# Performance work log

Measured on AMD Instinct MI355X. Metric: run time of the kernel, lower is better.

Reference implementation:

```python
import jax, jax.numpy as jnp
import numpy as np

N = 50000   # nodes
E = 600000  # edges
F = 128     # num_features
H = 128     # hidden_channels
G = 64      # graphs in batch


def setup_inputs() -> dict:
    key = jax.random.key(0)
    ks = jax.random.split(key, 12)
    x = jax.random.normal(ks[0], (N, F), dtype=jnp.float32)
    edge_index = jax.random.randint(ks[1], (2, E), 0, N, dtype=jnp.int64)
    edge_mask = jax.random.randint(ks[2], (E,), 0, 3, dtype=jnp.int64)
    batch = jnp.sort(jax.random.randint(ks[3], (N,), 0, G, dtype=jnp.int64))
    s = 0.05
    W1 = jax.random.normal(ks[4], (F, H), dtype=jnp.float32) * s
    b1 = jnp.zeros((H,), jnp.float32)
    W2 = jax.random.normal(ks[5], (H, H), dtype=jnp.float32) * s
    b2 = jnp.zeros((H,), jnp.float32)
    W3 = jax.random.normal(ks[6], (H, H), dtype=jnp.float32) * s
    b3 = jnp.zeros((H,), jnp.float32)
    Wl = jax.random.normal(ks[7], (H, 1), dtype=jnp.float32) * s
    bl = jnp.zeros((1,), jnp.float32)
    return {"x": x, "edge_index": edge_index, "edge_mask": edge_mask, "batch": batch,
            "W1": W1, "b1": b1, "W2": W2, "b2": b2, "W3": W3, "b3": b3, "Wl": Wl, "bl": bl}


def gcn_conv(x, W, b, src, dst, ew, n):
    """PyG GCNConv: add self-loops, symmetric deg^-1/2 normalization.
    ew is a {0,1} per-edge weight implementing the dynamic edge subset
    (equivalent to edge_index[:, idx] subsetting, since masked edges
    contribute neither to degree nor to aggregation)."""
    h = x @ W                                                # [n, H]
    deg = jax.ops.segment_sum(ew, dst, num_segments=n) + 1.0  # self-loop adds 1
    dinv = jax.lax.rsqrt(deg)                                # deg^-1/2
    norm = ew * dinv[src] * dinv[dst]                        # per-edge coeff
    agg = jax.ops.segment_sum(h[src] * norm[:, None], dst, num_segments=n)
    agg = agg + h * (dinv * dinv)[:, None]                   # self-loop term 1/deg_i
    return agg + b


def reference(x, edge_index, edge_mask, batch, W1, b1, W2, b2, W3, b3, Wl, bl):
    src, dst = edge_index[0], edge_index[1]
    ones = jnp.ones((E,), x.dtype)
    h = jax.nn.relu(gcn_conv(x, W1, b1, src, dst, ones, N))
    m1 = (edge_mask == 1).astype(x.dtype)
    h = jax.nn.relu(gcn_conv(h, W2, b2, src, dst, m1, N))
    m2 = (edge_mask == 2).astype(x.dtype)
    h = gcn_conv(h, W3, b3, src, dst, m2, N)
    # global_mean_pool over batch ids
    sums = jax.ops.segment_sum(h, batch, num_segments=G)        # [G, H]
    cnt = jax.ops.segment_sum(jnp.ones((N,), h.dtype), batch, num_segments=G)
    pooled = sums / jnp.clip(cnt, 1.0)[:, None]
    # dropout(p=0.3) is identity in eval mode
    return pooled @ Wl + bl
```

## Files before the change

kernel.cpp:

```cpp
#include <hip/hip_runtime.h>

#define NN 50000
#define EE 600000
#define HH 128
#define GG 64
#define NPAD 50176
#define NR 196
#define RN 256
#define EPB 3072
#define SCAP 3584
#define STAGB 7168
#define SC12 1536
#define CSR1OFF 702464
#define CSR2OFF 1003520

typedef __attribute__((ext_vector_type(8))) short short8;
typedef __attribute__((ext_vector_type(4))) float f32x4;
typedef __attribute__((ext_vector_type(4))) unsigned int u32x4;

__device__ __forceinline__ float bf2f(unsigned int u16) {
    union { unsigned int i; float f; } v; v.i = u16 << 16; return v.f;
}
__device__ __forceinline__ unsigned short f2bf(float f) {
    union { float f; unsigned int i; } v; v.f = f;
    unsigned int u = v.i;
    return (unsigned short)((u + 0x7FFFu + ((u >> 16) & 1u)) >> 16);
}

__device__ __forceinline__ short8 cvt8(f32x4 lo, f32x4 hi) {
    short8 r;
    r[0] = (short)f2bf(lo[0]); r[1] = (short)f2bf(lo[1]);
    r[2] = (short)f2bf(lo[2]); r[3] = (short)f2bf(lo[3]);
    r[4] = (short)f2bf(hi[0]); r[5] = (short)f2bf(hi[1]);
    r[6] = (short)f2bf(hi[2]); r[7] = (short)f2bf(hi[3]);
    return r;
}

__global__ void k_wt3z(const float* __restrict__ W1, const float* __restrict__ W2,
                       const float* __restrict__ W3, unsigned short* __restrict__ wt,
                       float* __restrict__ sums, int* __restrict__ scnt) {
    int i = blockIdx.x * 256 + threadIdx.x;
    if (i < GG * HH) sums[i] = 0.f;
    if (i < NR) scnt[i] = 0;
    int which = i >> 14;
    int r = i & 16383;
    const float* w = (which == 0) ? W1 : (which == 1) ? W2 : W3;
    int k = r >> 7, n = r & 127;
    wt[which * 16384 + n * HH + k] = f2bf(w[r]);
}

__global__ __launch_bounds__(256) void k_part(const int* __restrict__ ei, const int* __restrict__ mask,
                                              int* __restrict__ scnt, unsigned int* __restrict__ sbuf) {
    __shared__ int bcnt[256];
    __shared__ int bcur[256];
    __shared__ int gbase[256];
    int t = threadIdx.x;
    int e0 = blockIdx.x * EPB;
    unsigned int pk[12]; int bin[12];
    bcnt[t] = 0; bcur[t] = 0;
    __syncthreads();
    #pragma unroll
    for (int j = 0; j < 12; j++) {
        int e = e0 + j * 256 + t;
        if (e < EE) {
            int s = ei[e];
            int d = ei[EE + e];
            int m = mask[e];
            pk[j] = (unsigned int)s | ((unsigned int)(d & 255) << 16) | ((unsigned int)m << 24);
            bin[j] = d >> 8;
            atomicAdd(&bcnt[bin[j]], 1);
        } else bin[j] = -1;
    }
    __syncthreads();
    int v = bcnt[t];
    gbase[t] = (v > 0) ? atomicAdd(&scnt[t], v) : 0;
    __syncthreads();
    #pragma unroll
    for (int j = 0; j < 12; j++) {
        if (bin[j] >= 0) {
            int b = bin[j];
            int pos = gbase[b] + atomicAdd(&bcur[b], 1);
            if (pos < SCAP) sbuf[(size_t)b * SCAP + pos] = pk[j];
        }
    }
}

__global__ __launch_bounds__(256) void k_bld(const int* __restrict__ scnt,
                                             const unsigned int* __restrict__ sbuf,
                                             float* __restrict__ dinv,
                                             int* __restrict__ rpS, int* __restrict__ rpE,
                                             unsigned short* __restrict__ csr) {
    __shared__ int l0[RN], l1[RN], l2[RN];
    __shared__ int lrp0[RN], lrp1[RN], lrp2[RN];
    __shared__ int lc0[RN], lc1[RN], lc2[RN];
    __shared__ int wsum[12];
    __shared__ int ctot[3];
    __shared__ unsigned short stag[STAGB];
    int t = threadIdx.x, lane = t & 63, w = t >> 6;
    int rng = blockIdx.x;
    l0[t] = 0; l1[t] = 0; l2[t] = 0;
    lc0[t] = 0; lc1[t] = 0; lc2[t] = 0;
    __syncthreads();
    int cnt = scnt[rng]; if (cnt > SCAP) cnt = SCAP;
    const unsigned int* sb = sbuf + (size_t)rng * SCAP;
    for (int i = t; i < cnt; i += 256) {
        unsigned int p = sb[i];
        int dl = (int)((p >> 16) & 255u);
        int m = (int)(p >> 24);
        atomicAdd(&l0[dl], 1);
        if (m == 1) atomicAdd(&l1[dl], 1);
        else if (m == 2) atomicAdd(&l2[dl], 1);
    }
    __syncthreads();
    int a = l0[t], b = l1[t], c = l2[t];
    int x0 = a, x1 = b, x2 = c;
    #pragma unroll
    for (int off = 1; off < 64; off <<= 1) {
        int u0 = __shfl_up(x0, off), u1 = __shfl_up(x1, off), u2 = __shfl_up(x2, off);
        if (lane >= off) { x0 += u0; x1 += u1; x2 += u2; }
    }
    if (lane == 63) { wsum[w] = x0; wsum[4 + w] = x1; wsum[8 + w] = x2; }
    __syncthreads();
    int wo0 = 0, wo1 = 0, wo2 = 0;
    for (int k = 0; k < w; k++) { wo0 += wsum[k]; wo1 += wsum[4 + k]; wo2 += wsum[8 + k]; }
    int e0 = wo0 + x0 - a, e1 = wo1 + x1 - b, e2 = wo2 + x2 - c;
    lrp0[t] = e0; lrp1[t] = e1; lrp2[t] = e2;
    if (t == 255) { ctot[0] = e0 + a; ctot[1] = e1 + b; ctot[2] = e2 + c; }
    int node = rng * RN + t;
    dinv[node] = rsqrtf((float)a + 1.0f);
    dinv[NPAD + node] = rsqrtf((float)b + 1.0f);
    dinv[2 * NPAD + node] = rsqrtf((float)c + 1.0f);
    int base0 = rng * SCAP;
    int base1 = CSR1OFF + rng * SC12;
    int base2 = CSR2OFF + rng * SC12;
    rpS[node] = base0 + e0;            rpE[node] = base0 + e0 + a;
    rpS[NPAD + node] = base1 + e1;     rpE[NPAD + node] = base1 + e1 + b;
    rpS[2 * NPAD + node] = base2 + e2; rpE[2 * NPAD + node] = base2 + e2 + c;
    __syncthreads();
    int c0 = ctot[0], c1 = ctot[1], c2 = ctot[2];
    for (int i = t; i < cnt; i += 256) {
        unsigned int p = sb[i];
        unsigned short src = (unsigned short)(p & 0xffffu);
        int dl = (int)((p >> 16) & 255u);
        int m = (int)(p >> 24);
        int sl = lrp0[dl] + atomicAdd(&lc0[dl], 1);
        stag[sl] = src;
        if (m == 1) { sl = c0 + lrp1[dl] + atomicAdd(&lc1[dl], 1); stag[sl] = src; }
        else if (m == 2) { sl = c0 + c1 + lrp2[dl] + atomicAdd(&lc2[dl], 1); stag[sl] = src; }
    }
    __syncthreads();
    for (int i = t; i < c0; i += 256) csr[base0 + i] = stag[i];
    for (int i = t; i < c1; i += 256) csr[base1 + i] = stag[c0 + i];
    for (int i = t; i < c2; i += 256) csr[base2 + i] = stag[c0 + c1 + i];
}

__global__ __launch_bounds__(256) void k_gemm_f(const float* __restrict__ in,
                                                const unsigned short* __restrict__ wt,
                                                const float* __restrict__ dinv,
                                                unsigned short* __restrict__ h) {
    int w = threadIdx.x >> 6, lane = threadIdx.x & 63;
    int lr = lane & 15, lg = lane >> 4;
    int rowbase = (blockIdx.x * 4 + w) * 16;
    if (rowbase >= NN) return;
    int arow = rowbase + lr;
    const f32x4* ap = (const f32x4*)(in + (size_t)arow * HH + lg * 8);
    short8 a0 = cvt8(ap[0], ap[1]);
    short8 a1 = cvt8(ap[8], ap[9]);
    short8 a2 = cvt8(ap[16], ap[17]);
    short8 a3 = cvt8(ap[24], ap[25]);
    f32x4 acc[8];
    #pragma unroll
    for (int i = 0; i < 8; i++) acc[i] = (f32x4){0.f, 0.f, 0.f, 0.f};
    const unsigned short* wbase = wt + lr * HH + lg * 8;
    #pragma unroll
    for (int nc = 0; nc < 8; nc++) {
        const short8* bp = (const short8*)(wbase + nc * 16 * HH);
        short8 b0 = bp[0], b1 = bp[4], b2 = bp[8], b3 = bp[12];
        acc[nc] = __builtin_amdgcn_mfma_f32_16x16x32_bf16(a0, b0, acc[nc], 0, 0, 0);
        acc[nc] = __builtin_amdgcn_mfma_f32_16x16x32_bf16(a1, b1, acc[nc], 0, 0, 0);
        acc[nc] = __builtin_amdgcn_mfma_f32_16x16x32_bf16(a2, b2, acc[nc], 0, 0, 0);
        acc[nc] = __builtin_amdgcn_mfma_f32_16x16x32_bf16(a3, b3, acc[nc], 0, 0, 0);
    }
    int orow = rowbase + lg * 4;
    f32x4 dv = *(const f32x4*)(dinv + orow);
    #pragma unroll
    for (int nc = 0; nc < 8; nc++) {
        #pragma unroll
        for (int j = 0; j < 4; j++) {
            h[(size_t)(orow + j) * HH + nc * 16 + lr] = f2bf(acc[nc][j] * dv[j]);
        }
    }
}

__global__ __launch_bounds__(256) void k_gemm_b(const unsigned short* __restrict__ in,
                                                const unsigned short* __restrict__ wt,
                                                const float* __restrict__ dinv,
                                                unsigned short* __restrict__ h) {
    int w = threadIdx.x >> 6, lane = threadIdx.x & 63;
    int lr = lane & 15, lg = lane >> 4;
    int rowbase = (blockIdx.x * 4 + w) * 16;
    if (rowbase >= NN) return;
    int arow = rowbase + lr;
    const short8* ap = (const short8*)(in + (size_t)arow * HH + lg * 8);
    short8 a0 = ap[0], a1 = ap[4], a2 = ap[8], a3 = ap[12];
    f32x4 acc[8];
    #pragma unroll
    for (int i = 0; i < 8; i++) acc[i] = (f32x4){0.f, 0.f, 0.f, 0.f};
    const unsigned short* wbase = wt + lr * HH + lg * 8;
    #pragma unroll
    for (int nc = 0; nc < 8; nc++) {
        const short8* bp = (const short8*)(wbase + nc * 16 * HH);
        short8 b0 = bp[0], b1 = bp[4], b2 = bp[8], b3 = bp[12];
        acc[nc] = __builtin_amdgcn_mfma_f32_16x16x32_bf16(a0, b0, acc[nc], 0, 0, 0);
        acc[nc] = __builtin_amdgcn_mfma_f32_16x16x32_bf16(a1, b1, acc[nc], 0, 0, 0);
        acc[nc] = __builtin_amdgcn_mfma_f32_16x16x32_bf16(a2, b2, acc[nc], 0, 0, 0);
        acc[nc] = __builtin_amdgcn_mfma_f32_16x16x32_bf16(a3, b3, acc[nc], 0, 0, 0);
    }
    int orow = rowbase + lg * 4;
    f32x4 dv = *(const f32x4*)(dinv + orow);
    #pragma unroll
    for (int nc = 0; nc < 8; nc++) {
        #pragma unroll
        for (int j = 0; j < 4; j++) {
            h[(size_t)(orow + j) * HH + nc * 16 + lr] = f2bf(acc[nc][j] * dv[j]);
        }
    }
}

__global__ __launch_bounds__(256) void k_agg(const unsigned short* __restrict__ h,
                                             const float* __restrict__ dinv,
                                             const unsigned short* __restrict__ csr,
                                             const int* __restrict__ rpS,
                                             const int* __restrict__ rpE,
                                             const float* __restrict__ bias,
                                             unsigned short* __restrict__ g,
                                             int relu) {
    int tid = threadIdx.x;
    int n = blockIdx.x * 16 + (tid >> 4);
    int l = tid & 15;
    u32x4 hv = *(const u32x4*)(h + (size_t)n * HH + l * 8);
    float acc[8];
    #pragma unroll
    for (int q = 0; q < 4; q++) {
        acc[2*q] = bf2f(hv[q] & 0xffffu);
        acc[2*q+1] = bf2f(hv[q] >> 16);
    }
    int e = rpS[n], end = rpE[n];
    for (; e + 7 < end; e += 8) {
        int s0 = (int)csr[e],     s1 = (int)csr[e + 1], s2 = (int)csr[e + 2], s3 = (int)csr[e + 3];
        int s4 = (int)csr[e + 4], s5 = (int)csr[e + 5], s6 = (int)csr[e + 6], s7 = (int)csr[e + 7];
        u32x4 v0 = *(const u32x4*)(h + (size_t)s0 * HH + l * 8);
        u32x4 v1 = *(const u32x4*)(h + (size_t)s1 * HH + l * 8);
        u32x4 v2 = *(const u32x4*)(h + (size_t)s2 * HH + l * 8);
        u32x4 v3 = *(const u32x4*)(h + (size_t)s3 * HH + l * 8);
        u32x4 v4 = *(const u32x4*)(h + (size_t)s4 * HH + l * 8);
        u32x4 v5 = *(const u32x4*)(h + (size_t)s5 * HH + l * 8);
        u32x4 v6 = *(const u32x4*)(h + (size_t)s6 * HH + l * 8);
        u32x4 v7 = *(const u32x4*)(h + (size_t)s7 * HH + l * 8);
        #pragma unroll
        for (int q = 0; q < 4; q++) {
            acc[2*q] += bf2f(v0[q] & 0xffffu); acc[2*q+1] += bf2f(v0[q] >> 16);
            acc[2*q] += bf2f(v1[q] & 0xffffu); acc[2*q+1] += bf2f(v1[q] >> 16);
            acc[2*q] += bf2f(v2[q] & 0xffffu); acc[2*q+1] += bf2f(v2[q] >> 16);
            acc[2*q] += bf2f(v3[q] & 0xffffu); acc[2*q+1] += bf2f(v3[q] >> 16);
            acc[2*q] += bf2f(v4[q] & 0xffffu); acc[2*q+1] += bf2f(v4[q] >> 16);
            acc[2*q] += bf2f(v5[q] & 0xffffu); acc[2*q+1] += bf2f(v5[q] >> 16);
            acc[2*q] += bf2f(v6[q] & 0xffffu); acc[2*q+1] += bf2f(v6[q] >> 16);
            acc[2*q] += bf2f(v7[q] & 0xffffu); acc[2*q+1] += bf2f(v7[q] >> 16);
        }
    }
    for (; e + 3 < end; e += 4) {
        int s0 = (int)csr[e], s1 = (int)csr[e + 1], s2 = (int)csr[e + 2], s3 = (int)csr[e + 3];
        u32x4 v0 = *(const u32x4*)(h + (size_t)s0 * HH + l * 8);
        u32x4 v1 = *(const u32x4*)(h + (size_t)s1 * HH + l * 8);
        u32x4 v2 = *(const u32x4*)(h + (size_t)s2 * HH + l * 8);
        u32x4 v3 = *(const u32x4*)(h + (size_t)s3 * HH + l * 8);
        #pragma unroll
        for (int q = 0; q < 4; q++) {
            acc[2*q] += bf2f(v0[q] & 0xffffu); acc[2*q+1] += bf2f(v0[q] >> 16);
            acc[2*q] += bf2f(v1[q] & 0xffffu); acc[2*q+1] += bf2f(v1[q] >> 16);
            acc[2*q] += bf2f(v2[q] & 0xffffu); acc[2*q+1] += bf2f(v2[q] >> 16);
            acc[2*q] += bf2f(v3[q] & 0xffffu); acc[2*q+1] += bf2f(v3[q] >> 16);
        }
    }
    for (; e < end; e++) {
        int s0 = (int)csr[e];
        u32x4 v0 = *(const u32x4*)(h + (size_t)s0 * HH + l * 8);
        #pragma unroll
        for (int q = 0; q < 4; q++) {
            acc[2*q] += bf2f(v0[q] & 0xffffu); acc[2*q+1] += bf2f(v0[q] >> 16);
        }
    }
    float di = dinv[n];
    f32x4 bp0 = *(const f32x4*)(bias + l * 8);
    f32x4 bp1 = *(const f32x4*)(bias + l * 8 + 4);
    float bb[8] = {bp0[0], bp0[1], bp0[2], bp0[3], bp1[0], bp1[1], bp1[2], bp1[3]};
    #pragma unroll
    for (int q = 0; q < 8; q++) {
        acc[q] = acc[q] * di + bb[q];
        if (relu) acc[q] = fmaxf(acc[q], 0.f);
    }
    u32x4 o;
    #pragma unroll
    for (int q = 0; q < 4; q++)
        o[q] = (unsigned int)f2bf(acc[2*q]) | ((unsigned int)f2bf(acc[2*q+1]) << 16);
    *(u32x4*)(g + (size_t)n * HH + l * 8) = o;
}

__global__ __launch_bounds__(128) void k_pool_part(const unsigned short* __restrict__ g3,
                                                   const int* __restrict__ batch,
                                                   float* __restrict__ sums) {
    int t = threadIdx.x;
    int n0 = blockIdx.x * 64;
    int n1 = n0 + 64; if (n1 > NN) n1 = NN;
    int curb = batch[n0];
    float acc = 0.f;
    for (int n = n0; n < n1; n++) {
        int b = batch[n];
        if (b != curb) {
            atomicAdd(&sums[curb * HH + t], acc);
            acc = 0.f;
            curb = b;
        }
        acc += bf2f((unsigned int)g3[(size_t)n * HH + t]);
    }
    atomicAdd(&sums[curb * HH + t], acc);
}

__device__ __forceinline__ int lbound(const int* a, int n, int key) {
    int lo = 0, hi = n;
    while (lo < hi) { int mid = (lo + hi) >> 1; if (a[mid] < key) lo = mid + 1; else hi = mid; }
    return lo;
}

__global__ __launch_bounds__(128) void k_head(const float* __restrict__ sums,
                                              const int* __restrict__ batch,
                                              const float* __restrict__ Wl,
                                              const float* __restrict__ bl,
                                              float* __restrict__ out) {
    int gid = blockIdx.x;
    int t = threadIdx.x;
    int lo = lbound(batch, NN, gid);
    int hi = lbound(batch, NN, gid + 1);
    float cnt = (float)(hi - lo);
    if (cnt < 1.f) cnt = 1.f;
    float prod = (sums[gid * HH + t] / cnt) * Wl[t];
    __shared__ float sm[128];
    sm[t] = prod;
    __syncthreads();
    for (int off = 64; off > 0; off >>= 1) {
        if (t < off) sm[t] += sm[t + off];
        __syncthreads();
    }
    if (t == 0) out[gid] = sm[0] + bl[0];
}

extern "C" void kernel_launch(void* const* d_in, const int* in_sizes, int n_in,
                              void* d_out, int out_size, void* d_ws, size_t ws_size,
                              hipStream_t stream) {
    const float* x    = (const float*)d_in[0];
    const int*   ei   = (const int*)d_in[1];
    const int*   mask = (const int*)d_in[2];
    const int*   batch= (const int*)d_in[3];
    const float* W1   = (const float*)d_in[4];
    const float* b1   = (const float*)d_in[5];
    const float* W2   = (const float*)d_in[6];
    const float* b2   = (const float*)d_in[7];
    const float* W3   = (const float*)d_in[8];
    const float* b3   = (const float*)d_in[9];
    const float* Wl   = (const float*)d_in[10];
    const float* bl   = (const float*)d_in[11];
    float* out = (float*)d_out;

    char* ws = (char*)d_ws;
    unsigned short* g = (unsigned short*)(ws + 0);
    unsigned short* h = (unsigned short*)(ws + 12800000);
    unsigned short* wt1 = (unsigned short*)(ws + 25600000);
    unsigned short* wt2 = wt1 + 16384;
    unsigned short* wt3 = wt2 + 16384;
    float* dinv= (float*)(ws + 25698304);
    int* rpS   = (int*)(ws + 26300416);
    int* rpE   = (int*)(ws + 26902528);
    int* scnt  = (int*)(ws + 27504640);
    unsigned short* csr = (unsigned short*)(ws + 27505664);
    unsigned int* sbuf = (unsigned int*)(ws + 30114816);
    float* sums = (float*)(ws + 32924672);

    float* dinv1 = dinv;
    float* dinv2 = dinv + NPAD;
    float* dinv3 = dinv + 2 * NPAD;

    dim3 b256(256);
    k_wt3z<<<dim3(192), b256, 0, stream>>>(W1, W2, W3, wt1, sums, scnt);
    k_part<<<dim3((EE + EPB - 1) / EPB), b256, 0, stream>>>(ei, mask, scnt, sbuf);
    k_bld<<<dim3(NR), b256, 0, stream>>>(scnt, sbuf, dinv, rpS, rpE, csr);

    dim3 ggrid((NN + 63) / 64);
    dim3 agrid(NN / 16);

    k_gemm_f<<<ggrid, b256, 0, stream>>>(x, wt1, dinv1, h);
    k_agg<<<agrid, b256, 0, stream>>>(h, dinv1, csr, rpS, rpE, b1, g, 1);
    k_gemm_b<<<ggrid, b256, 0, stream>>>(g, wt2, dinv2, h);
    k_agg<<<agrid, b256, 0, stream>>>(h, dinv2, csr, rpS + NPAD, rpE + NPAD, b2, g, 1);
    k_gemm_b<<<ggrid, b256, 0, stream>>>(g, wt3, dinv3, h);
    k_agg<<<agrid, b256, 0, stream>>>(h, dinv3, csr, rpS + 2 * NPAD, rpE + 2 * NPAD, b3, g, 0);

    k_pool_part<<<dim3((NN + 63) / 64), dim3(128), 0, stream>>>(g, batch, sums);
    k_head<<<dim3(GG), dim3(128), 0, stream>>>(sums, batch, Wl, bl, out);
}
```

Before: 182.5 us.

## Fuse aggregation with the following layer's GEMM via shared-memory tile

Layers 1 and 2 now aggregate neighbours, apply bias and ReLU, and stage the 16-row result in shared memory. The same block then runs the next layer's MFMA GEMM on that tile and writes the dinv-scaled output directly. This drops two separate GEMM launches and the round trip of the intermediate activation through global memory. The costs are a block barrier after the irregular gather phase, more shared memory per block, and a smaller GEMM tile per block, with W reloaded per block.

Measured after the change: 160.0 us (median of 2 runs). 12.3% less time.

```diff
diff --git a/kernel.cpp b/kernel.cpp
--- a/kernel.cpp
+++ b/kernel.cpp
@@ -13,6 +13,7 @@
 #define SC12 1536
 #define CSR1OFF 702464
 #define CSR2OFF 1003520
+#define GTS 138
 
 typedef __attribute__((ext_vector_type(8))) short short8;
 typedef __attribute__((ext_vector_type(4))) float f32x4;
@@ -192,60 +193,9 @@
     }
 }
 
-__global__ __launch_bounds__(256) void k_gemm_b(const unsigned short* __restrict__ in,
-                                                const unsigned short* __restrict__ wt,
-                                                const float* __restrict__ dinv,
-                                                unsigned short* __restrict__ h) {
-    int w = threadIdx.x >> 6, lane = threadIdx.x & 63;
-    int lr = lane & 15, lg = lane >> 4;
-    int rowbase = (blockIdx.x * 4 + w) * 16;
-    if (rowbase >= NN) return;
-    int arow = rowbase + lr;
-    const short8* ap = (const short8*)(in + (size_t)arow * HH + lg * 8);
-    short8 a0 = ap[0], a1 = ap[4], a2 = ap[8], a3 = ap[12];
-    f32x4 acc[8];
-    #pragma unroll
-    for (int i = 0; i < 8; i++) acc[i] = (f32x4){0.f, 0.f, 0.f, 0.f};
-    const unsigned short* wbase = wt + lr * HH + lg * 8;
-    #pragma unroll
-    for (int nc = 0; nc < 8; nc++) {
-        const short8* bp = (const short8*)(wbase + nc * 16 * HH);
-        short8 b0 = bp[0], b1 = bp[4], b2 = bp[8], b3 = bp[12];
-        acc[nc] = __builtin_amdgcn_mfma_f32_16x16x32_bf16(a0, b0, acc[nc], 0, 0, 0);
-        acc[nc] = __builtin_amdgcn_mfma_f32_16x16x32_bf16(a1, b1, acc[nc], 0, 0, 0);
-        acc[nc] = __builtin_amdgcn_mfma_f32_16x16x32_bf16(a2, b2, acc[nc], 0, 0, 0);
-        acc[nc] = __builtin_amdgcn_mfma_f32_16x16x32_bf16(a3, b3, acc[nc], 0, 0, 0);
-    }
-    int orow = rowbase + lg * 4;
-    f32x4 dv = *(const f32x4*)(dinv + orow);
-    #pragma unroll
-    for (int nc = 0; nc < 8; nc++) {
-        #pragma unroll
-        for (int j = 0; j < 4; j++) {
-            h[(size_t)(orow + j) * HH + nc * 16 + lr] = f2bf(acc[nc][j] * dv[j]);
-        }
-    }
-}
-
-__global__ __launch_bounds__(256) void k_agg(const unsigned short* __restrict__ h,
-                                             const float* __restrict__ dinv,
-                                             const unsigned short* __restrict__ csr,
-                                             const int* __restrict__ rpS,
-                                             const int* __restrict__ rpE,
-                                             const float* __restrict__ bias,
-                                             unsigned short* __restrict__ g,
-                                             int relu) {
-    int tid = threadIdx.x;
-    int n = blockIdx.x * 16 + (tid >> 4);
-    int l = tid & 15;
-    u32x4 hv = *(const u32x4*)(h + (size_t)n * HH + l * 8);
-    float acc[8];
-    #pragma unroll
-    for (int q = 0; q < 4; q++) {
-        acc[2*q] = bf2f(hv[q] & 0xffffu);
-        acc[2*q+1] = bf2f(hv[q] >> 16);
-    }
-    int e = rpS[n], end = rpE[n];
+__device__ __forceinline__ void agg_edges(const unsigned short* __restrict__ h,
+                                          const unsigned short* __restrict__ csr,
+                                          int e, int end, int l, float* acc) {
     for (; e + 7 < end; e += 8) {
         int s0 = (int)csr[e],     s1 = (int)csr[e + 1], s2 = (int)csr[e + 2], s3 = (int)csr[e + 3];
         int s4 = (int)csr[e + 4], s5 = (int)csr[e + 5], s6 = (int)csr[e + 6], s7 = (int)csr[e + 7];
@@ -291,19 +241,101 @@
             acc[2*q] += bf2f(v0[q] & 0xffffu); acc[2*q+1] += bf2f(v0[q] >> 16);
         }
     }
+}
+
+__global__ __launch_bounds__(256) void k_aggemm(const unsigned short* __restrict__ h,
+                                                const float* __restrict__ dinvA,
+                                                const unsigned short* __restrict__ csr,
+                                                const int* __restrict__ rpS,
+                                                const int* __restrict__ rpE,
+                                                const float* __restrict__ bias,
+                                                const unsigned short* __restrict__ wt,
+                                                const float* __restrict__ dinvB,
+                                                unsigned short* __restrict__ hout) {
+    __shared__ unsigned short gt[16][GTS];
+    int tid = threadIdx.x;
+    int n0 = blockIdx.x * 16;
+    int nl = tid >> 4;
+    int n = n0 + nl;
+    int l = tid & 15;
+    u32x4 hv = *(const u32x4*)(h + (size_t)n * HH + l * 8);
+    float acc[8];
+    #pragma unroll
+    for (int q = 0; q < 4; q++) {
+        acc[2*q] = bf2f(hv[q] & 0xffffu);
+        acc[2*q+1] = bf2f(hv[q] >> 16);
+    }
+    agg_edges(h, csr, rpS[n], rpE[n], l, acc);
+    float di = dinvA[n];
+    f32x4 bp0 = *(const f32x4*)(bias + l * 8);
+    f32x4 bp1 = *(const f32x4*)(bias + l * 8 + 4);
+    float bb[8] = {bp0[0], bp0[1], bp0[2], bp0[3], bp1[0], bp1[1], bp1[2], bp1[3]};
+    #pragma unroll
+    for (int q = 0; q < 8; q++) {
+        float v = fmaxf(acc[q] * di + bb[q], 0.f);
+        gt[nl][l * 8 + q] = f2bf(v);
+    }
+    __syncthreads();
+    int lane = tid & 63, w = tid >> 6;
+    int lr = lane & 15, lg = lane >> 4;
+    short8 a0 = *(const short8*)&gt[lr][lg * 8];
+    short8 a1 = *(const short8*)&gt[lr][32 + lg * 8];
+    short8 a2 = *(const short8*)&gt[lr][64 + lg * 8];
+    short8 a3 = *(const short8*)&gt[lr][96 + lg * 8];
+    f32x4 oacc[2];
+    oacc[0] = (f32x4){0.f, 0.f, 0.f, 0.f};
+    oacc[1] = (f32x4){0.f, 0.f, 0.f, 0.f};
+    #pragma unroll
+    for (int nc2 = 0; nc2 < 2; nc2++) {
+        int nc = w * 2 + nc2;
+        const short8* bp = (const short8*)(wt + (nc * 16 + lr) * HH + lg * 8);
+        short8 b0 = bp[0], b1 = bp[4], b2 = bp[8], b3 = bp[12];
+        oacc[nc2] = __builtin_amdgcn_mfma_f32_16x16x32_bf16(a0, b0, oacc[nc2], 0, 0, 0);
+        oacc[nc2] = __builtin_amdgcn_mfma_f32_16x16x32_bf16(a1, b1, oacc[nc2], 0, 0, 0);
+        oacc[nc2] = __builtin_amdgcn_mfma_f32_16x16x32_bf16(a2, b2, oacc[nc2], 0, 0, 0);
+        oacc[nc2] = __builtin_amdgcn_mfma_f32_16x16x32_bf16(a3, b3, oacc[nc2], 0, 0, 0);
+    }
+    int orow = n0 + lg * 4;
+    f32x4 dv = *(const f32x4*)(dinvB + orow);
+    #pragma unroll
+    for (int nc2 = 0; nc2 < 2; nc2++) {
+        int nc = w * 2 + nc2;
+        #pragma unroll
+        for (int j = 0; j < 4; j++) {
+            hout[(size_t)(orow + j) * HH + nc * 16 + lr] = f2bf(oacc[nc2][j] * dv[j]);
+        }
+    }
+}
+
+__global__ __launch_bounds__(256) void k_agg(const unsigned short* __restrict__ h,
+                                             const float* __restrict__ dinv,
+                                             const unsigned short* __restrict__ csr,
+                                             const int* __restrict__ rpS,
+                                             const int* __restrict__ rpE,
+                                             const float* __restrict__ bias,
+                                             unsigned short* __restrict__ g) {
+    int tid = threadIdx.x;
+    int n = blockIdx.x * 16 + (tid >> 4);
+    int l = tid & 15;
+    u32x4 hv = *(const u32x4*)(h + (size_t)n * HH + l * 8);
+    float acc[8];
+    #pragma unroll
+    for (int q = 0; q < 4; q++) {
+        acc[2*q] = bf2f(hv[q] & 0xffffu);
+        acc[2*q+1] = bf2f(hv[q] >> 16);
+    }
+    agg_edges(h, csr, rpS[n], rpE[n], l, acc);
     float di = dinv[n];
     f32x4 bp0 = *(const f32x4*)(bias + l * 8);
     f32x4 bp1 = *(const f32x4*)(bias + l * 8 + 4);
     float bb[8] = {bp0[0], bp0[1], bp0[2], bp0[3], bp1[0], bp1[1], bp1[2], bp1[3]};
-    #pragma unroll
-    for (int q = 0; q < 8; q++) {
-        acc[q] = acc[q] * di + bb[q];
-        if (relu) acc[q] = fmaxf(acc[q], 0.f);
-    }
     u32x4 o;
     #pragma unroll
-    for (int q = 0; q < 4; q++)
-        o[q] = (unsigned int)f2bf(acc[2*q]) | ((unsigned int)f2bf(acc[2*q+1]) << 16);
+    for (int q = 0; q < 4; q++) {
+        float v0 = acc[2*q] * di + bb[2*q];
+        float v1 = acc[2*q+1] * di + bb[2*q+1];
+        o[q] = (unsigned int)f2bf(v0) | ((unsigned int)f2bf(v1) << 16);
+    }
     *(u32x4*)(g + (size_t)n * HH + l * 8) = o;
 }
 
@@ -399,11 +431,9 @@
     dim3 agrid(NN / 16);
 
     k_gemm_f<<<ggrid, b256, 0, stream>>>(x, wt1, dinv1, h);
-    k_agg<<<agrid, b256, 0, stream>>>(h, dinv1, csr, rpS, rpE, b1, g, 1);
-    k_gemm_b<<<ggrid, b256, 0, stream>>>(g, wt2, dinv2, h);
-    k_agg<<<agrid, b256, 0, stream>>>(h, dinv2, csr, rpS + NPAD, rpE + NPAD, b2, g, 1);
-    k_gemm_b<<<ggrid, b256, 0, stream>>>(g, wt3, dinv3, h);
-    k_agg<<<agrid, b256, 0, stream>>>(h, dinv3, csr, rpS + 2 * NPAD, rpE + 2 * NPAD, b3, g, 0);
+    k_aggemm<<<agrid, b256, 0, stream>>>(h, dinv1, csr, rpS, rpE, b1, wt2, dinv2, g);
+    k_aggemm<<<agrid, b256, 0, stream>>>(g, dinv2, csr, rpS + NPAD, rpE + NPAD, b2, wt3, dinv3, h);
+    k_agg<<<agrid, b256, 0, stream>>>(h, dinv3, csr, rpS + 2 * NPAD, rpE + 2 * NPAD, b3, g);
 
     k_pool_part<<<dim3((NN + 63) / 64), dim3(128), 0, stream>>>(g, batch, sums);
     k_head<<<dim3(GG), dim3(128), 0, stream>>>(sums, batch, Wl, bl, out);
```
